# Optimization experiments

Hardware: AMD Instinct MI355X
Metric: run time of the kernel (lower is better)

## Reference

```python
import jax, jax.numpy as jnp
import numpy as np

EMBED_DIM = 512
N_HEADS = 16
HEAD_DIM = EMBED_DIM // N_HEADS  # 32


def setup_inputs() -> dict:
    key0 = jax.random.key(0)
    ks = jax.random.split(key0, 8)
    B, S, D = 4, 2048, EMBED_DIM
    inp = {
        "key": jax.random.normal(ks[0], (B, S, D), dtype=jnp.float32),
        "query": jax.random.normal(ks[1], (B, S, D), dtype=jnp.float32),
        "value": jax.random.normal(ks[2], (B, S, D), dtype=jnp.float32),
        # per-head projection weights (nn.Linear: y = x @ W.T), no bias
        "Wq": jax.random.normal(ks[3], (HEAD_DIM, HEAD_DIM), dtype=jnp.float32) * 0.1,
        "Wk": jax.random.normal(ks[4], (HEAD_DIM, HEAD_DIM), dtype=jnp.float32) * 0.1,
        "Wv": jax.random.normal(ks[5], (HEAD_DIM, HEAD_DIM), dtype=jnp.float32) * 0.1,
        # output projection with bias
        "Wo": jax.random.normal(ks[6], (EMBED_DIM, EMBED_DIM), dtype=jnp.float32) * 0.05,
        "bo": jax.random.normal(ks[7], (EMBED_DIM,), dtype=jnp.float32) * 0.01,
    }
    return inp


def reference(key, query, value, Wq, Wk, Wv, Wo, bo):
    B, S, D = key.shape
    Sq = query.shape[1]
    H, dh = N_HEADS, HEAD_DIM
    # reshape to [B, S, H, dh] then per-head linear (x @ W.T)
    k = jnp.einsum('bshd,ed->bhse', key.reshape(B, S, H, dh), Wk)
    q = jnp.einsum('bshd,ed->bhse', query.reshape(B, Sq, H, dh), Wq)
    v = jnp.einsum('bshd,ed->bhse', value.reshape(B, S, H, dh), Wv)
    # naive attention: full [B,H,Sq,S] scores
    scores = jnp.einsum('bhqd,bhkd->bhqk', q, k) / jnp.sqrt(jnp.float32(dh))
    attn = jax.nn.softmax(scores, axis=-1)
    ctx = jnp.einsum('bhqk,bhkd->bhqd', attn, v)  # [B,H,Sq,dh]
    concat = ctx.transpose(0, 2, 1, 3).reshape(B, Sq, H * dh)
    return concat @ Wo.T + bo
```

## Files before the change

### kernel.cpp

```cpp
#include <hip/hip_runtime.h>
#include <hip/hip_bf16.h>


typedef __attribute__((ext_vector_type(8))) short bf16x8;
typedef __attribute__((ext_vector_type(4))) float f32x4;

#define MFMA16(a, b, c) __builtin_amdgcn_mfma_f32_16x16x32_bf16(a, b, c, 0, 0, 0)

static __device__ __forceinline__ unsigned short f2bf(float f) {
  __bf16 h = (__bf16)f;
  union { __bf16 h; unsigned short u; } c; c.h = h; return c.u;
}
static __device__ __forceinline__ float bf2f(unsigned short u) {
  union { unsigned u; float f; } c; c.u = ((unsigned)u) << 16; return c.f;
}

static __device__ __forceinline__ void gld_lds16(const ushort* g, ushort* l) {
  __builtin_amdgcn_global_load_lds(
      (const __attribute__((address_space(1))) unsigned int*)g,
      (__attribute__((address_space(3))) unsigned int*)l, 16, 0, 0);
}

static __device__ __forceinline__ void load8_split(const float* p, bf16x8& hi, bf16x8& lo) {
  float4 a = *(const float4*)p;
  float4 b = *(const float4*)(p + 4);
  float v[8] = {a.x, a.y, a.z, a.w, b.x, b.y, b.z, b.w};
  #pragma unroll
  for (int j = 0; j < 8; ++j) {
    unsigned short h = f2bf(v[j]);
    hi[j] = (short)h;
    lo[j] = (short)f2bf(v[j] - bf2f(h));
  }
}

__global__ __launch_bounds__(256) void proj_kernel(
    const float* __restrict__ key, const float* __restrict__ query,
    const float* __restrict__ value,
    const float* __restrict__ Wq, const float* __restrict__ Wk,
    const float* __restrict__ Wv, const float* __restrict__ Wo,
    ushort* __restrict__ Qp, ushort* __restrict__ Kp, ushort* __restrict__ Vt,
    ushort* __restrict__ Wob) {
  if (blockIdx.x >= 2048) {
    int i = ((blockIdx.x - 2048) * 256 + threadIdx.x) * 4;
    float4 v = *(const float4*)&Wo[i];
    ushort4 o;
    o.x = f2bf(v.x); o.y = f2bf(v.y); o.z = f2bf(v.z); o.w = f2bf(v.w);
    *(ushort4*)&Wob[i] = o;
    return;
  }
  __shared__ ushort tlds[4][16][40];
  const int tid = threadIdx.x;
  const int l = tid & 63, wid = tid >> 6;
  const int lr = l & 15, lc = l >> 4;
  const int task = blockIdx.x * 4 + wid;
  const int h = task & 15;
  const int st = (task >> 4) & 127;
  const int b = task >> 11;
  const int bh = b * 16 + h;
  const size_t xoff = ((size_t)b * 2048 + st * 16 + lr) * 512 + h * 32 + lc * 8;
  const float ALPHA = 0.2550354039f;

  #pragma unroll
  for (int t = 0; t < 3; ++t) {
    const float* x = (t == 0) ? query : (t == 1) ? key : value;
    const float* W = (t == 0) ? Wq : (t == 1) ? Wk : Wv;
    bf16x8 xh, xl;
    load8_split(x + xoff, xh, xl);
    f32x4 accs[2];
    #pragma unroll
    for (int eh = 0; eh < 2; ++eh) {
      bf16x8 wh, wl;
      load8_split(W + (size_t)(eh * 16 + lr) * 32 + lc * 8, wh, wl);
      f32x4 acc = {0.f, 0.f, 0.f, 0.f};
      acc = MFMA16(xh, wh, acc);
      acc = MFMA16(xh, wl, acc);
      acc = MFMA16(xl, wh, acc);
      accs[eh] = acc;
    }
    if (t == 2) {
      #pragma unroll
      for (int eh = 0; eh < 2; ++eh) {
        ushort4 pk;
        pk.x = f2bf(accs[eh][0]); pk.y = f2bf(accs[eh][1]);
        pk.z = f2bf(accs[eh][2]); pk.w = f2bf(accs[eh][3]);
        *(ushort4*)&Vt[((size_t)bh * 32 + eh * 16 + lr) * 2048 + st * 16 + lc * 4] = pk;
      }
    } else {
      const float scale = (t == 0) ? ALPHA : 1.0f;
      #pragma unroll
      for (int eh = 0; eh < 2; ++eh)
        #pragma unroll
        for (int r = 0; r < 4; ++r)
          tlds[wid][lc * 4 + r][eh * 16 + lr] = f2bf(accs[eh][r] * scale);
      bf16x8 row = *(const bf16x8*)&tlds[wid][l >> 2][(l & 3) * 8];
      ushort* dst = ((t == 0) ? Qp : Kp) +
                    ((size_t)bh * 2048 + st * 16 + (l >> 2)) * 32 + (l & 3) * 8;
      *(bf16x8*)dst = row;
    }
  }
}

__global__ __launch_bounds__(512) void attn_kernel(
    const ushort* __restrict__ Qp, const ushort* __restrict__ Kp,
    const ushort* __restrict__ Vt, ushort* __restrict__ Cb) {
  __shared__ ushort kv[3][4096];
  const int tid = threadIdx.x;
  const int l = tid & 63, w = tid >> 6;
  const int lr = l & 15, lc = l >> 4;
  const int xcd = blockIdx.x & 7, idx = blockIdx.x >> 3;
  const int bh = xcd * 8 + (idx >> 3);
  const int qblk = idx & 7;
  const int b = bh >> 4, h = bh & 15;
  const int q0 = qblk * 256 + w * 32;

  const ushort* Qb = Qp + (size_t)bh * 2048 * 32;
  const ushort* Kb = Kp + (size_t)bh * 2048 * 32;
  const ushort* Vb = Vt + (size_t)bh * 32 * 2048;

  const bool stageK = tid < 256;
  const int st = stageK ? tid : tid - 256;
  const int si = st ^ ((st >> 3) & 7);
  const int m = si >> 2, pp = si & 3;
  const int g = (m & 32) | ((m & 12) << 1) | ((m & 16) >> 2) | (m & 3);
  const ushort* src0 = stageK
      ? Kb + (size_t)(g * 4 + pp) * 8
      : Vb + (size_t)(st >> 3) * 2048 + (((st & 7) ^ ((st >> 3) & 7)) * 8);
  const size_t sstep = stageK ? (size_t)64 * 32 : (size_t)64;
  const int dofs = (stageK ? 0 : 2048) + st * 8;

  int koff[4];
  #pragma unroll
  for (int kg = 0; kg < 4; ++kg) {
    int v = (kg * 16 + lr) * 4 + lc;
    v ^= (v >> 3) & 7;
    koff[kg] = v * 8;
  }
  int voff[2][2];
  #pragma unroll
  for (int kc = 0; kc < 2; ++kc)
    #pragma unroll
    for (int eh = 0; eh < 2; ++eh) {
      int v = (eh * 16 + lr) * 8 + kc * 4 + lc;
      v ^= (v >> 3) & 7;
      voff[kc][eh] = 2048 + v * 8;
    }

  bf16x8 qf[2];
  qf[0] = *(const bf16x8*)&Qb[(size_t)(q0 + lr) * 32 + lc * 8];
  qf[1] = *(const bf16x8*)&Qb[(size_t)(q0 + 16 + lr) * 32 + lc * 8];

  bf16x8 ones;
  #pragma unroll
  for (int j = 0; j < 8; ++j) ones[j] = (short)0x3F80;

  f32x4 octx[2][2] = {};
  f32x4 dacc[2] = {};
  const f32x4 zero = {0.f, 0.f, 0.f, 0.f};

  gld_lds16(src0, &kv[0][dofs]);
  gld_lds16(src0 + sstep, &kv[1][dofs]);
  asm volatile("s_waitcnt vmcnt(1)" ::: "memory");
  __builtin_amdgcn_s_barrier();

  int cur = 0, nx2 = 2;
  for (int kt = 0; kt < 32; ++kt) {
    if (kt < 30)
      gld_lds16(src0 + (size_t)(kt + 2) * sstep, &kv[nx2][dofs]);

    const ushort* kb = kv[cur];
    bf16x8 kf[4];
    #pragma unroll
    for (int kg = 0; kg < 4; ++kg)
      kf[kg] = *(const bf16x8*)&kb[koff[kg]];
    bf16x8 vf[2][2];
    #pragma unroll
    for (int kc = 0; kc < 2; ++kc)
      #pragma unroll
      for (int eh = 0; eh < 2; ++eh)
        vf[kc][eh] = *(const bf16x8*)&kb[voff[kc][eh]];

    #pragma unroll
    for (int qi = 0; qi < 2; ++qi) {
      f32x4 sc[4];
      #pragma unroll
      for (int kg = 0; kg < 4; ++kg)
        sc[kg] = MFMA16(kf[kg], qf[qi], zero);
      #pragma unroll
      for (int kc = 0; kc < 2; ++kc) {
        bf16x8 pa;
        #pragma unroll
        for (int r = 0; r < 4; ++r) {
          pa[r]     = (short)f2bf(__builtin_amdgcn_exp2f(sc[2 * kc][r]));
          pa[4 + r] = (short)f2bf(__builtin_amdgcn_exp2f(sc[2 * kc + 1][r]));
        }
        #pragma unroll
        for (int eh = 0; eh < 2; ++eh)
          octx[qi][eh] = MFMA16(pa, vf[kc][eh], octx[qi][eh]);
        dacc[qi] = MFMA16(pa, ones, dacc[qi]);
      }
    }

    if (kt < 30) {
      asm volatile("s_waitcnt vmcnt(1)" ::: "memory");
    } else {
      asm volatile("s_waitcnt vmcnt(0)" ::: "memory");
    }
    __builtin_amdgcn_s_barrier();
    cur = (cur == 2) ? 0 : cur + 1;
    nx2 = (nx2 == 2) ? 0 : nx2 + 1;
  }

  #pragma unroll
  for (int qi = 0; qi < 2; ++qi) {
    float inv[4];
    #pragma unroll
    for (int r = 0; r < 4; ++r)
      inv[r] = 1.0f / dacc[qi][r];
    #pragma unroll
    for (int eh = 0; eh < 2; ++eh)
      #pragma unroll
      for (int r = 0; r < 4; ++r) {
        float v = octx[qi][eh][r] * inv[r];
        Cb[((size_t)b * 2048 + q0 + qi * 16 + lc * 4 + r) * 512 + h * 32 + eh * 16 + lr] =
            f2bf(v);
      }
  }
}

__global__ __launch_bounds__(256) void oproj_kernel(
    const ushort* __restrict__ Cb, const ushort* __restrict__ Wob,
    const float* __restrict__ bo, float* __restrict__ out) {
  const int tid = threadIdx.x;
  const int l = tid & 63, w = tid >> 6;
  const int lr = l & 15, lc = l >> 4;
  const int qt = blockIdx.x >> 1;
  const int nt = blockIdx.x & 1;
  const int r0 = qt * 64;
  const int n0 = nt * 256 + w * 64;

  f32x4 acc[4][4] = {};
  for (int kk = 0; kk < 16; ++kk) {
    const int k0 = kk * 32;
    bf16x8 af[4], bf[4];
    #pragma unroll
    for (int i = 0; i < 4; ++i)
      af[i] = *(const bf16x8*)&Cb[(size_t)(r0 + i * 16 + lr) * 512 + k0 + lc * 8];
    #pragma unroll
    for (int j = 0; j < 4; ++j)
      bf[j] = *(const bf16x8*)&Wob[(size_t)(n0 + j * 16 + lr) * 512 + k0 + lc * 8];
    #pragma unroll
    for (int i = 0; i < 4; ++i)
      #pragma unroll
      for (int j = 0; j < 4; ++j)
        acc[i][j] = MFMA16(af[i], bf[j], acc[i][j]);
  }
  #pragma unroll
  for (int j = 0; j < 4; ++j) {
    float bias = bo[n0 + j * 16 + lr];
    #pragma unroll
    for (int i = 0; i < 4; ++i)
      #pragma unroll
      for (int r = 0; r < 4; ++r)
        out[(size_t)(r0 + i * 16 + lc * 4 + r) * 512 + n0 + j * 16 + lr] =
            acc[i][j][r] + bias;
  }
}

extern "C" void kernel_launch(void* const* d_in, const int* in_sizes, int n_in,
                              void* d_out, int out_size, void* d_ws, size_t ws_size,
                              hipStream_t stream) {
  (void)in_sizes; (void)n_in; (void)out_size; (void)ws_size;
  const float* key   = (const float*)d_in[0];
  const float* query = (const float*)d_in[1];
  const float* value = (const float*)d_in[2];
  const float* Wq    = (const float*)d_in[3];
  const float* Wk    = (const float*)d_in[4];
  const float* Wv    = (const float*)d_in[5];
  const float* Wo    = (const float*)d_in[6];
  const float* bo    = (const float*)d_in[7];
  float* out = (float*)d_out;

  const size_t NT = (size_t)4 * 16 * 2048 * 32;
  ushort* ws  = (ushort*)d_ws;
  ushort* Qp  = ws;
  ushort* Kp  = Qp + NT;
  ushort* Vt  = Kp + NT;
  ushort* Cb  = Vt + NT;
  ushort* Wob = Cb + NT;

  hipLaunchKernelGGL(proj_kernel, dim3(2304), dim3(256), 0, stream,
                     key, query, value, Wq, Wk, Wv, Wo, Qp, Kp, Vt, Wob);
  hipLaunchKernelGGL(attn_kernel, dim3(512), dim3(512), 0, stream, Qp, Kp, Vt, Cb);
  hipLaunchKernelGGL(oproj_kernel, dim3(256), dim3(256), 0, stream, Cb, Wob, bo, out);
}
```

Before: 89.81 us.

## Fuse Q projection into attention kernel, drop Qp workspace round trip

```diff
diff --git a/kernel.cpp b/kernel.cpp
--- a/kernel.cpp
+++ b/kernel.cpp
@@ -34,12 +34,10 @@
 }
 
 __global__ __launch_bounds__(256) void proj_kernel(
-    const float* __restrict__ key, const float* __restrict__ query,
-    const float* __restrict__ value,
-    const float* __restrict__ Wq, const float* __restrict__ Wk,
-    const float* __restrict__ Wv, const float* __restrict__ Wo,
-    ushort* __restrict__ Qp, ushort* __restrict__ Kp, ushort* __restrict__ Vt,
-    ushort* __restrict__ Wob) {
+    const float* __restrict__ key, const float* __restrict__ value,
+    const float* __restrict__ Wk, const float* __restrict__ Wv,
+    const float* __restrict__ Wo,
+    ushort* __restrict__ Kp, ushort* __restrict__ Vt, ushort* __restrict__ Wob) {
   if (blockIdx.x >= 2048) {
     int i = ((blockIdx.x - 2048) * 256 + threadIdx.x) * 4;
     float4 v = *(const float4*)&Wo[i];
@@ -58,12 +56,11 @@
   const int b = task >> 11;
   const int bh = b * 16 + h;
   const size_t xoff = ((size_t)b * 2048 + st * 16 + lr) * 512 + h * 32 + lc * 8;
-  const float ALPHA = 0.2550354039f;
-
-  #pragma unroll
-  for (int t = 0; t < 3; ++t) {
-    const float* x = (t == 0) ? query : (t == 1) ? key : value;
-    const float* W = (t == 0) ? Wq : (t == 1) ? Wk : Wv;
+
+  #pragma unroll
+  for (int t = 1; t < 3; ++t) {
+    const float* x = (t == 1) ? key : value;
+    const float* W = (t == 1) ? Wk : Wv;
     bf16x8 xh, xl;
     load8_split(x + xoff, xh, xl);
     f32x4 accs[2];
@@ -86,24 +83,24 @@
         *(ushort4*)&Vt[((size_t)bh * 32 + eh * 16 + lr) * 2048 + st * 16 + lc * 4] = pk;
       }
     } else {
-      const float scale = (t == 0) ? ALPHA : 1.0f;
       #pragma unroll
       for (int eh = 0; eh < 2; ++eh)
         #pragma unroll
         for (int r = 0; r < 4; ++r)
-          tlds[wid][lc * 4 + r][eh * 16 + lr] = f2bf(accs[eh][r] * scale);
+          tlds[wid][lc * 4 + r][eh * 16 + lr] = f2bf(accs[eh][r]);
       bf16x8 row = *(const bf16x8*)&tlds[wid][l >> 2][(l & 3) * 8];
-      ushort* dst = ((t == 0) ? Qp : Kp) +
-                    ((size_t)bh * 2048 + st * 16 + (l >> 2)) * 32 + (l & 3) * 8;
+      ushort* dst = Kp + ((size_t)bh * 2048 + st * 16 + (l >> 2)) * 32 + (l & 3) * 8;
       *(bf16x8*)dst = row;
     }
   }
 }
 
 __global__ __launch_bounds__(512) void attn_kernel(
-    const ushort* __restrict__ Qp, const ushort* __restrict__ Kp,
-    const ushort* __restrict__ Vt, ushort* __restrict__ Cb) {
+    const float* __restrict__ query, const float* __restrict__ Wq,
+    const ushort* __restrict__ Kp, const ushort* __restrict__ Vt,
+    ushort* __restrict__ Cb) {
   __shared__ ushort kv[3][4096];
+  __shared__ ushort qscr[8][640];
   const int tid = threadIdx.x;
   const int l = tid & 63, w = tid >> 6;
   const int lr = l & 15, lc = l >> 4;
@@ -112,10 +109,36 @@
   const int qblk = idx & 7;
   const int b = bh >> 4, h = bh & 15;
   const int q0 = qblk * 256 + w * 32;
-
-  const ushort* Qb = Qp + (size_t)bh * 2048 * 32;
+  const float ALPHA = 0.2550354039f;
+
   const ushort* Kb = Kp + (size_t)bh * 2048 * 32;
   const ushort* Vb = Vt + (size_t)bh * 32 * 2048;
+
+  bf16x8 qf[2];
+  {
+    ushort* scr = qscr[w];
+    bf16x8 wh[2], wl[2];
+    #pragma unroll
+    for (int eh = 0; eh < 2; ++eh)
+      load8_split(Wq + (size_t)(eh * 16 + lr) * 32 + lc * 8, wh[eh], wl[eh]);
+    #pragma unroll
+    for (int qi = 0; qi < 2; ++qi) {
+      const float* xq = query + ((size_t)b * 2048 + q0 + qi * 16 + lr) * 512 + h * 32 + lc * 8;
+      bf16x8 xh, xl;
+      load8_split(xq, xh, xl);
+      #pragma unroll
+      for (int eh = 0; eh < 2; ++eh) {
+        f32x4 acc = {0.f, 0.f, 0.f, 0.f};
+        acc = MFMA16(xh, wh[eh], acc);
+        acc = MFMA16(xh, wl[eh], acc);
+        acc = MFMA16(xl, wh[eh], acc);
+        #pragma unroll
+        for (int r = 0; r < 4; ++r)
+          scr[(lc * 4 + r) * 40 + eh * 16 + lr] = f2bf(acc[r] * ALPHA);
+      }
+      qf[qi] = *(const bf16x8*)&scr[lr * 40 + lc * 8];
+    }
+  }
 
   const bool stageK = tid < 256;
   const int st = stageK ? tid : tid - 256;
@@ -145,10 +168,6 @@
       voff[kc][eh] = 2048 + v * 8;
     }
 
-  bf16x8 qf[2];
-  qf[0] = *(const bf16x8*)&Qb[(size_t)(q0 + lr) * 32 + lc * 8];
-  qf[1] = *(const bf16x8*)&Qb[(size_t)(q0 + 16 + lr) * 32 + lc * 8];
-
   bf16x8 ones;
   #pragma unroll
   for (int j = 0; j < 8; ++j) ones[j] = (short)0x3F80;
@@ -159,7 +178,7 @@
 
   gld_lds16(src0, &kv[0][dofs]);
   gld_lds16(src0 + sstep, &kv[1][dofs]);
-  asm volatile("s_waitcnt vmcnt(1)" ::: "memory");
+  asm volatile("s_waitcnt vmcnt(0)" ::: "memory");
   __builtin_amdgcn_s_barrier();
 
   int cur = 0, nx2 = 2;
@@ -282,14 +301,14 @@
 
   const size_t NT = (size_t)4 * 16 * 2048 * 32;
   ushort* ws  = (ushort*)d_ws;
-  ushort* Qp  = ws;
-  ushort* Kp  = Qp + NT;
+  ushort* Kp  = ws;
   ushort* Vt  = Kp + NT;
   ushort* Cb  = Vt + NT;
   ushort* Wob = Cb + NT;
 
   hipLaunchKernelGGL(proj_kernel, dim3(2304), dim3(256), 0, stream,
-                     key, query, value, Wq, Wk, Wv, Wo, Qp, Kp, Vt, Wob);
-  hipLaunchKernelGGL(attn_kernel, dim3(512), dim3(512), 0, stream, Qp, Kp, Vt, Cb);
+                     key, value, Wk, Wv, Wo, Kp, Vt, Wob);
+  hipLaunchKernelGGL(attn_kernel, dim3(512), dim3(512), 0, stream,
+                     query, Wq, Kp, Vt, Cb);
   hipLaunchKernelGGL(oproj_kernel, dim3(256), dim3(256), 0, stream, Cb, Wob, bo, out);
 }
```

Result: slower. 92.08 us (+2.5%).
